# Performance work log

Hardware: AMD Instinct MI355X
Metric: run time of the kernel (lower is better)

The kernel has to match this reference:

```python
import jax, jax.numpy as jnp
import numpy as np
from jax import lax

B, T, D_IN, D_OUT = 8, 4096, 256, 256


def setup_inputs() -> dict:
    key = jax.random.key(0)
    k1, k2, k3, k4, k5 = jax.random.split(key, 5)
    bound_in = 1.0 / np.sqrt(D_IN)
    return {
        "inputs": jax.random.normal(k1, (B, T, D_IN), dtype=jnp.float32),
        "mask": jnp.zeros((B, T, 1), dtype=jnp.float32),
        "W_in": jax.random.uniform(k2, (D_OUT, D_IN), jnp.float32, -bound_in, bound_in),
        "b_in": jax.random.uniform(k3, (D_OUT,), jnp.float32, -bound_in, bound_in),
        "W_f": jax.random.uniform(k4, (D_OUT, D_IN), jnp.float32, -bound_in, bound_in),
        "b_f": jax.random.uniform(k5, (D_OUT,), jnp.float32, -bound_in, bound_in),
    }


def _forget_mult(f, x):
    # h_t = f_t * x_t + (1 - f_t) * h_{t-1}, h_{-1} = 0 (torchqrnn ForgetMult, hidden_init=None)
    fT = jnp.swapaxes(f, 0, 1)  # (T, B, D)
    xT = jnp.swapaxes(x, 0, 1)

    def step(h, fx):
        ft, xt = fx
        h = ft * xt + (1.0 - ft) * h
        return h, h

    h0 = jnp.zeros(xT.shape[1:], dtype=x.dtype)  # (B, D)
    _, hs = lax.scan(step, h0, (fT, xT))
    return jnp.swapaxes(hs, 0, 1)  # (B, T, D)


def reference(inputs, mask, W_in, b_in, W_f, b_f):
    # right_to_left = False -> no flips
    x = jnp.tanh(jnp.einsum("btd,od->bto", inputs, W_in) + b_in)
    f = jax.nn.sigmoid(jnp.einsum("btd,od->bto", inputs, W_f) + b_f + mask * 10000.0)
    return _forget_mult(f, x)
```

## Files before the change

### kernel.cpp

```cpp
#include <hip/hip_runtime.h>
#include <math.h>


typedef _Float16 f16x8 __attribute__((ext_vector_type(8)));
typedef float f32x4 __attribute__((ext_vector_type(4)));
typedef float f32x16 __attribute__((ext_vector_type(16)));
typedef unsigned int u32x4 __attribute__((ext_vector_type(4)));

constexpr int B_ = 8, T_ = 4096, D_ = 256, K_ = 256;
constexpr int M_ = B_ * T_;
constexpr int CHUNK = 64;
constexpr int NCH = T_ / CHUNK;
constexpr int NBLK = M_ / CHUNK;
constexpr int SLICE_EL = 8192;

struct alignas(4) XF { _Float16 x, f; };
struct alignas(4) HP2 { _Float16 h, p; };
union UHP { unsigned int u; HP2 hp; XF xf; };

__device__ __forceinline__ float fexp2(float a) { return __builtin_amdgcn_exp2f(a); }
__device__ __forceinline__ float frcp(float a) { return __builtin_amdgcn_rcpf(a); }
constexpr float L2E = 1.4426950408889634f;

__device__ __forceinline__ float fast_sigmoid(float z) {
  return frcp(1.f + fexp2(-z * L2E));
}
__device__ __forceinline__ float fast_tanh(float z) {
  const float t = fexp2(-2.f * L2E * fabsf(z));
  return copysignf((1.f - t) * frcp(1.f + t), z);
}

__global__ __launch_bounds__(256) void wconv(const float* __restrict__ Win,
                                             const float* __restrict__ Wf,
                                             _Float16* __restrict__ Wh2) {
  const int t = blockIdx.x * 256 + threadIdx.x;
  const int n = t & 255;
  const int kc = (t >> 8) & 1;
  const int mat = (t >> 9) & 1;
  const int kk2 = t >> 10;
  const float* s = (mat ? Wf : Win) + (size_t)n * K_ + kk2 * 16 + kc * 8;
  f32x4 a = *(const f32x4*)s;
  f32x4 b = *(const f32x4*)(s + 4);
  f16x8 o;
  o[0] = (_Float16)a[0]; o[1] = (_Float16)a[1];
  o[2] = (_Float16)a[2]; o[3] = (_Float16)a[3];
  o[4] = (_Float16)b[0]; o[5] = (_Float16)b[1];
  o[6] = (_Float16)b[2]; o[7] = (_Float16)b[3];
  *(f16x8*)(Wh2 + (size_t)t * 8) = o;
}

__global__ __launch_bounds__(256, 3) void gemm_hp(
    const float* __restrict__ A, const _Float16* __restrict__ Wh2,
    const float* __restrict__ bin, const float* __restrict__ bfv,
    const float* __restrict__ mask, unsigned int* __restrict__ HPout,
    float* __restrict__ Ap, float* __restrict__ Hp) {
  __shared__ __align__(16) char smem[32768];
  char* ldsA = smem;

  const int tid = threadIdx.x;
  const int w = tid >> 6, lane = tid & 63;
  const int mw = w >> 1, nw = w & 1;
  const int nl = lane & 31, kh = lane >> 5;
  const int ml = mw * 32 + nl;
  const int g = blockIdx.x;
  const int row0 = g * CHUNK;

  f32x16 acc[2][4];
#pragma unroll
  for (int mat = 0; mat < 2; ++mat)
#pragma unroll
    for (int nt = 0; nt < 4; ++nt) acc[mat][nt] = (f32x16)(0.f);

  {
    const int am = tid >> 2;
    const int ak4 = (tid & 3) * 8;
    const float* agp = A + (size_t)(row0 + am) * K_ + ak4 * 8;
#pragma unroll
    for (int j = 0; j < 8; ++j) {
      const int kcg = ak4 + j;
      f32x4 lo = *(const f32x4*)(agp + j * 8);
      f32x4 hi = *(const f32x4*)(agp + j * 8 + 4);
      f16x8 t;
      t[0] = (_Float16)lo[0]; t[1] = (_Float16)lo[1];
      t[2] = (_Float16)lo[2]; t[3] = (_Float16)lo[3];
      t[4] = (_Float16)hi[0]; t[5] = (_Float16)hi[1];
      t[6] = (_Float16)hi[2]; t[7] = (_Float16)hi[3];
      *(f16x8*)(ldsA + am * 512 + ((kcg ^ (am & 31)) << 4)) = t;
    }
  }
  __syncthreads();

  for (int kk2 = 0; kk2 < 16; ++kk2) {
    f16x8 afr;
    {
      const int kcg = kk2 * 2 + kh;
      afr = *(const f16x8*)(ldsA + ml * 512 + ((kcg ^ (ml & 31)) << 4));
    }
    const _Float16* wslice = Wh2 + (size_t)kk2 * SLICE_EL;
#pragma unroll
    for (int mat = 0; mat < 2; ++mat)
#pragma unroll
      for (int nt = 0; nt < 4; ++nt) {
        const int n = nw * 128 + nt * 32 + nl;
        f16x8 bfr = *(const f16x8*)(wslice + (size_t)((mat * 2 + kh) * 256 + n) * 8);
        acc[mat][nt] = __builtin_amdgcn_mfma_f32_32x32x16_f16(
            afr, bfr, acc[mat][nt], 0, 0, 0);
      }
  }
  __syncthreads();

  float bx[4], bf[4];
#pragma unroll
  for (int nt = 0; nt < 4; ++nt) {
    const int col = nw * 128 + nt * 32 + nl;
    bx[nt] = bin[col];
    bf[nt] = bfv[col];
  }
  float madd[16];
#pragma unroll
  for (int reg = 0; reg < 16; ++reg) {
    const int rl = mw * 32 + (reg & 3) + 8 * (reg >> 2) + 4 * kh;
    madd[reg] = 10000.f * mask[row0 + rl];
  }

  const int d = tid;
  float hrun = 0.f, Prun = 1.f;
#pragma unroll
  for (int p = 0; p < 2; ++p) {
    if (mw == p) {
#pragma unroll
      for (int nt = 0; nt < 4; ++nt) {
        const int col = nw * 128 + nt * 32 + nl;
#pragma unroll
        for (int reg = 0; reg < 16; ++reg) {
          const int rloc = (reg & 3) + 8 * (reg >> 2) + 4 * kh;
          const float zx = acc[0][nt][reg] + bx[nt];
          const float zf = acc[1][nt][reg] + bf[nt] + madd[reg];
          XF v;
          v.x = (_Float16)fast_tanh(zx);
          v.f = (_Float16)fast_sigmoid(zf);
          *(XF*)(smem + ((size_t)rloc * D_ + col) * 4) = v;
        }
      }
    }
    __syncthreads();
#pragma unroll 8
    for (int t = 0; t < 32; ++t) {
      char* slot = smem + ((size_t)t * D_ + d) * 4;
      const XF v = *(const XF*)slot;
      const float f = (float)v.f;
      const float a = 1.f - f;
      hrun = f * (float)v.x + a * hrun;
      Prun *= a;
      HP2 o;
      o.h = (_Float16)hrun;
      o.p = (_Float16)Prun;
      *(HP2*)slot = o;
    }
    __syncthreads();
#pragma unroll
    for (int j = 0; j < 8; ++j) {
      const int c = j * 256 + tid;
      u32x4 vv = *(const u32x4*)(smem + (size_t)c * 16);
      *(u32x4*)(HPout + (size_t)g * 16384 + (size_t)p * 8192 + (size_t)c * 4) = vv;
    }
    __syncthreads();
  }

  Ap[(size_t)g * D_ + d] = Prun;
  Hp[(size_t)g * D_ + d] = hrun;
}

__global__ __launch_bounds__(256) void scan_mid(const float* __restrict__ Ap,
                                                const float* __restrict__ Hp,
                                                float* __restrict__ hs) {
  const int b = blockIdx.x, d = threadIdx.x;
  float h = 0.f;
#pragma unroll 8
  for (int c = 0; c < NCH; ++c) {
    const size_t i = ((size_t)(b * NCH + c)) * D_ + d;
    hs[i] = h;
    h = Hp[i] + Ap[i] * h;
  }
}

__global__ __launch_bounds__(256) void final_k(const unsigned int* __restrict__ HP,
                                               const float* __restrict__ hs,
                                               float* __restrict__ out) {
  const int g = blockIdx.x;
  const int lane = threadIdx.x & 63, wv = threadIdx.x >> 6;
  const int d0 = lane * 4;
  const f32x4 h0 = *(const f32x4*)(hs + (size_t)g * D_ + d0);
#pragma unroll 4
  for (int tt = 0; tt < 16; ++tt) {
    const int t = wv * 16 + tt;
    const size_t idx = ((size_t)g * CHUNK + t) * D_ + d0;
    u32x4 u = *(const u32x4*)(HP + idx);
    f32x4 o;
#pragma unroll
    for (int i = 0; i < 4; ++i) {
      UHP q; q.u = u[i];
      o[i] = (float)q.hp.h + (float)q.hp.p * h0[i];
    }
    *(f32x4*)(out + idx) = o;
  }
}

extern "C" void kernel_launch(void* const* d_in, const int* in_sizes, int n_in,
                              void* d_out, int out_size, void* d_ws, size_t ws_size,
                              hipStream_t stream) {
  const float* inputs = (const float*)d_in[0];
  const float* mask   = (const float*)d_in[1];
  const float* W_in   = (const float*)d_in[2];
  const float* b_in   = (const float*)d_in[3];
  const float* W_f    = (const float*)d_in[4];
  const float* b_f    = (const float*)d_in[5];
  float* out = (float*)d_out;
  char* ws = (char*)d_ws;

  constexpr size_t HPSZ = (size_t)M_ * D_ * 4;
  constexpr size_t WSZ  = (size_t)2 * 256 * 256 * 2;
  constexpr size_t SUM  = (size_t)NBLK * D_ * sizeof(float);

  unsigned int* HPb = (unsigned int*)ws;
  _Float16* Wh2 = (_Float16*)(ws + HPSZ);
  float* Ap = (float*)(ws + HPSZ + WSZ);
  float* Hp = (float*)(ws + HPSZ + WSZ + SUM);
  float* hs = (float*)(ws + HPSZ + WSZ + 2 * SUM);

  wconv<<<64, 256, 0, stream>>>(W_in, W_f, Wh2);
  gemm_hp<<<NBLK, 256, 0, stream>>>(inputs, Wh2, b_in, b_f, mask, HPb, Ap, Hp);
  scan_mid<<<B_, 256, 0, stream>>>(Ap, Hp, hs);
  final_k<<<NBLK, 256, 0, stream>>>(HPb, hs, out);
}
```

Baseline: 151.3 us.

## Fuse GEMM, chunk scan and fixup into one kernel with flag-based lookback

Merges the GEMM/chunk-scan, the cross-chunk scan and the final fixup into one kernel. Each block publishes its chunk carry through global flags, then waits for earlier chunks of the same sequence and recomputes its start state. This removes the large fp16 (h,p) intermediate round-trip through global memory. It also stages weight slices through LDS with register prefetch, and LDS doubles to 64KB, lowering occupancy to 2 blocks per CU. Spin-waiting assumes earlier blocks are scheduled first, which risks deadlock and serialization, and each block re-reads up to 63 prior carries.

Result: slower. 191.8 us (+26.8%).

```diff
diff --git a/kernel.cpp b/kernel.cpp
--- a/kernel.cpp
+++ b/kernel.cpp
@@ -32,8 +32,10 @@
 
 __global__ __launch_bounds__(256) void wconv(const float* __restrict__ Win,
                                              const float* __restrict__ Wf,
-                                             _Float16* __restrict__ Wh2) {
+                                             _Float16* __restrict__ Wh2,
+                                             int* __restrict__ flags) {
   const int t = blockIdx.x * 256 + threadIdx.x;
+  if (t < NBLK) flags[t] = 0;
   const int n = t & 255;
   const int kc = (t >> 8) & 1;
   const int mat = (t >> 9) & 1;
@@ -49,13 +51,15 @@
   *(f16x8*)(Wh2 + (size_t)t * 8) = o;
 }
 
-__global__ __launch_bounds__(256, 3) void gemm_hp(
+__global__ __launch_bounds__(256, 2) void fused(
     const float* __restrict__ A, const _Float16* __restrict__ Wh2,
     const float* __restrict__ bin, const float* __restrict__ bfv,
-    const float* __restrict__ mask, unsigned int* __restrict__ HPout,
-    float* __restrict__ Ap, float* __restrict__ Hp) {
-  __shared__ __align__(16) char smem[32768];
+    const float* __restrict__ mask, float* __restrict__ Ap,
+    float* __restrict__ Hp, int* __restrict__ flags,
+    float* __restrict__ out) {
+  __shared__ __align__(16) char smem[65536];
   char* ldsA = smem;
+  char* ldsW = smem + 32768;
 
   const int tid = threadIdx.x;
   const int w = tid >> 6, lane = tid & 63;
@@ -88,26 +92,40 @@
       *(f16x8*)(ldsA + am * 512 + ((kcg ^ (am & 31)) << 4)) = t;
     }
   }
+
+  f16x8 wreg[4];
+#pragma unroll
+  for (int j = 0; j < 4; ++j)
+    wreg[j] = *(const f16x8*)(Wh2 + (size_t)(j * 256 + tid) * 8);
   __syncthreads();
 
   for (int kk2 = 0; kk2 < 16; ++kk2) {
+#pragma unroll
+    for (int j = 0; j < 4; ++j)
+      *(f16x8*)(ldsW + (size_t)(j * 256 + tid) * 16) = wreg[j];
+    if (kk2 < 15) {
+#pragma unroll
+      for (int j = 0; j < 4; ++j)
+        wreg[j] = *(const f16x8*)(Wh2 + (size_t)(kk2 + 1) * SLICE_EL +
+                                  (size_t)(j * 256 + tid) * 8);
+    }
+    __syncthreads();
     f16x8 afr;
     {
       const int kcg = kk2 * 2 + kh;
       afr = *(const f16x8*)(ldsA + ml * 512 + ((kcg ^ (ml & 31)) << 4));
     }
-    const _Float16* wslice = Wh2 + (size_t)kk2 * SLICE_EL;
 #pragma unroll
     for (int mat = 0; mat < 2; ++mat)
 #pragma unroll
       for (int nt = 0; nt < 4; ++nt) {
         const int n = nw * 128 + nt * 32 + nl;
-        f16x8 bfr = *(const f16x8*)(wslice + (size_t)((mat * 2 + kh) * 256 + n) * 8);
+        f16x8 bfr = *(const f16x8*)(ldsW + (size_t)((mat * 2 + kh) * 256 + n) * 16);
         acc[mat][nt] = __builtin_amdgcn_mfma_f32_32x32x16_f16(
             afr, bfr, acc[mat][nt], 0, 0, 0);
       }
-  }
-  __syncthreads();
+    __syncthreads();
+  }
 
   float bx[4], bf[4];
 #pragma unroll
@@ -123,86 +141,78 @@
     madd[reg] = 10000.f * mask[row0 + rl];
   }
 
+#pragma unroll
+  for (int nt = 0; nt < 4; ++nt) {
+    const int col = nw * 128 + nt * 32 + nl;
+#pragma unroll
+    for (int reg = 0; reg < 16; ++reg) {
+      const int rloc = mw * 32 + (reg & 3) + 8 * (reg >> 2) + 4 * kh;
+      const float zx = acc[0][nt][reg] + bx[nt];
+      const float zf = acc[1][nt][reg] + bf[nt] + madd[reg];
+      XF v;
+      v.x = (_Float16)fast_tanh(zx);
+      v.f = (_Float16)fast_sigmoid(zf);
+      *(XF*)(smem + ((size_t)rloc * D_ + col) * 4) = v;
+    }
+  }
+  __syncthreads();
+
   const int d = tid;
   float hrun = 0.f, Prun = 1.f;
-#pragma unroll
-  for (int p = 0; p < 2; ++p) {
-    if (mw == p) {
-#pragma unroll
-      for (int nt = 0; nt < 4; ++nt) {
-        const int col = nw * 128 + nt * 32 + nl;
-#pragma unroll
-        for (int reg = 0; reg < 16; ++reg) {
-          const int rloc = (reg & 3) + 8 * (reg >> 2) + 4 * kh;
-          const float zx = acc[0][nt][reg] + bx[nt];
-          const float zf = acc[1][nt][reg] + bf[nt] + madd[reg];
-          XF v;
-          v.x = (_Float16)fast_tanh(zx);
-          v.f = (_Float16)fast_sigmoid(zf);
-          *(XF*)(smem + ((size_t)rloc * D_ + col) * 4) = v;
-        }
-      }
-    }
-    __syncthreads();
 #pragma unroll 8
-    for (int t = 0; t < 32; ++t) {
-      char* slot = smem + ((size_t)t * D_ + d) * 4;
-      const XF v = *(const XF*)slot;
-      const float f = (float)v.f;
-      const float a = 1.f - f;
-      hrun = f * (float)v.x + a * hrun;
-      Prun *= a;
-      HP2 o;
-      o.h = (_Float16)hrun;
-      o.p = (_Float16)Prun;
-      *(HP2*)slot = o;
-    }
-    __syncthreads();
-#pragma unroll
-    for (int j = 0; j < 8; ++j) {
-      const int c = j * 256 + tid;
-      u32x4 vv = *(const u32x4*)(smem + (size_t)c * 16);
-      *(u32x4*)(HPout + (size_t)g * 16384 + (size_t)p * 8192 + (size_t)c * 4) = vv;
-    }
-    __syncthreads();
-  }
-
+  for (int t = 0; t < 64; ++t) {
+    char* slot = smem + ((size_t)t * D_ + d) * 4;
+    const XF v = *(const XF*)slot;
+    const float f = (float)v.f;
+    const float a = 1.f - f;
+    hrun = f * (float)v.x + a * hrun;
+    Prun *= a;
+    HP2 o;
+    o.h = (_Float16)hrun;
+    o.p = (_Float16)Prun;
+    *(HP2*)slot = o;
+  }
   Ap[(size_t)g * D_ + d] = Prun;
   Hp[(size_t)g * D_ + d] = hrun;
-}
-
-__global__ __launch_bounds__(256) void scan_mid(const float* __restrict__ Ap,
-                                                const float* __restrict__ Hp,
-                                                float* __restrict__ hs) {
-  const int b = blockIdx.x, d = threadIdx.x;
-  float h = 0.f;
-#pragma unroll 8
-  for (int c = 0; c < NCH; ++c) {
-    const size_t i = ((size_t)(b * NCH + c)) * D_ + d;
-    hs[i] = h;
-    h = Hp[i] + Ap[i] * h;
-  }
-}
-
-__global__ __launch_bounds__(256) void final_k(const unsigned int* __restrict__ HP,
-                                               const float* __restrict__ hs,
-                                               float* __restrict__ out) {
-  const int g = blockIdx.x;
-  const int lane = threadIdx.x & 63, wv = threadIdx.x >> 6;
-  const int d0 = lane * 4;
-  const f32x4 h0 = *(const f32x4*)(hs + (size_t)g * D_ + d0);
+
+  __syncthreads();
+  __threadfence();
+  if (tid == 0)
+    __hip_atomic_store(flags + g, 1, __ATOMIC_RELEASE,
+                       __HIP_MEMORY_SCOPE_AGENT);
+
+  const int c = g & (NCH - 1);
+  const int g0 = g & ~(NCH - 1);
+  if (tid < c) {
+    while (__hip_atomic_load(flags + g0 + tid, __ATOMIC_ACQUIRE,
+                             __HIP_MEMORY_SCOPE_AGENT) == 0)
+      __builtin_amdgcn_s_sleep(2);
+  }
+  __syncthreads();
+  __threadfence();
+
+  const int wv = tid >> 6;
+  const int d0 = (tid & 63) * 4;
+  const size_t seqbase = (size_t)g0 * D_ + d0;
+  f32x4 h0 = (f32x4)(0.f);
+#pragma unroll 4
+  for (int j = 0; j < c; ++j) {
+    const f32x4 a4 = *(const f32x4*)(Ap + seqbase + (size_t)j * D_);
+    const f32x4 hh = *(const f32x4*)(Hp + seqbase + (size_t)j * D_);
+    h0 = hh + a4 * h0;
+  }
+
 #pragma unroll 4
   for (int tt = 0; tt < 16; ++tt) {
     const int t = wv * 16 + tt;
-    const size_t idx = ((size_t)g * CHUNK + t) * D_ + d0;
-    u32x4 u = *(const u32x4*)(HP + idx);
+    const u32x4 u = *(const u32x4*)(smem + ((size_t)t * D_ + d0) * 4);
     f32x4 o;
 #pragma unroll
     for (int i = 0; i < 4; ++i) {
       UHP q; q.u = u[i];
       o[i] = (float)q.hp.h + (float)q.hp.p * h0[i];
     }
-    *(f32x4*)(out + idx) = o;
+    *(f32x4*)(out + ((size_t)(row0 + t)) * D_ + d0) = o;
   }
 }
 
@@ -218,18 +228,15 @@
   float* out = (float*)d_out;
   char* ws = (char*)d_ws;
 
-  constexpr size_t HPSZ = (size_t)M_ * D_ * 4;
-  constexpr size_t WSZ  = (size_t)2 * 256 * 256 * 2;
-  constexpr size_t SUM  = (size_t)NBLK * D_ * sizeof(float);
-
-  unsigned int* HPb = (unsigned int*)ws;
-  _Float16* Wh2 = (_Float16*)(ws + HPSZ);
-  float* Ap = (float*)(ws + HPSZ + WSZ);
-  float* Hp = (float*)(ws + HPSZ + WSZ + SUM);
-  float* hs = (float*)(ws + HPSZ + WSZ + 2 * SUM);
-
-  wconv<<<64, 256, 0, stream>>>(W_in, W_f, Wh2);
-  gemm_hp<<<NBLK, 256, 0, stream>>>(inputs, Wh2, b_in, b_f, mask, HPb, Ap, Hp);
-  scan_mid<<<B_, 256, 0, stream>>>(Ap, Hp, hs);
-  final_k<<<NBLK, 256, 0, stream>>>(HPb, hs, out);
-}
+  constexpr size_t WSZ = (size_t)2 * 256 * 256 * 2;
+  constexpr size_t SUM = (size_t)NBLK * D_ * sizeof(float);
+
+  _Float16* Wh2 = (_Float16*)ws;
+  float* Ap = (float*)(ws + WSZ);
+  float* Hp = (float*)(ws + WSZ + SUM);
+  int* flags = (int*)(ws + WSZ + 2 * SUM);
+
+  wconv<<<64, 256, 0, stream>>>(W_in, W_f, Wh2, flags);
+  fused<<<NBLK, 256, 0, stream>>>(inputs, Wh2, b_in, b_f, mask, Ap, Hp,
+                                  flags, out);
+}
```

## Halve chunk size, stage weights via LDS, fold carry scan into final kernel

Applied to the files above, without the earlier changes.

Shrinks the time chunk from 64 to 32 rows so each GEMM block handles one 32-row tile, with each wave covering 64 output columns. Weight slices are staged through LDS using register prefetch, with occupancy raised to 4 blocks per CU. The separate 8-block serial scan_mid kernel is removed. Each final block instead recomputes its incoming carry by serially combining all previous chunk summaries. That removes a low-parallelism launch but adds redundant work, up to 127 sequential steps in late chunks, plus extra per-slice barriers in the GEMM.

Measured after the change: 140.7 us. -7.0%, faster.

```diff
diff --git a/kernel.cpp b/kernel.cpp
--- a/kernel.cpp
+++ b/kernel.cpp
@@ -9,7 +9,7 @@
 
 constexpr int B_ = 8, T_ = 4096, D_ = 256, K_ = 256;
 constexpr int M_ = B_ * T_;
-constexpr int CHUNK = 64;
+constexpr int CHUNK = 32;
 constexpr int NCH = T_ / CHUNK;
 constexpr int NBLK = M_ / CHUNK;
 constexpr int SLICE_EL = 8192;
@@ -49,34 +49,33 @@
   *(f16x8*)(Wh2 + (size_t)t * 8) = o;
 }
 
-__global__ __launch_bounds__(256, 3) void gemm_hp(
+__global__ __launch_bounds__(256, 4) void gemm_hp(
     const float* __restrict__ A, const _Float16* __restrict__ Wh2,
     const float* __restrict__ bin, const float* __restrict__ bfv,
     const float* __restrict__ mask, unsigned int* __restrict__ HPout,
     float* __restrict__ Ap, float* __restrict__ Hp) {
   __shared__ __align__(16) char smem[32768];
   char* ldsA = smem;
+  char* ldsW = smem + 16384;
 
   const int tid = threadIdx.x;
   const int w = tid >> 6, lane = tid & 63;
-  const int mw = w >> 1, nw = w & 1;
   const int nl = lane & 31, kh = lane >> 5;
-  const int ml = mw * 32 + nl;
   const int g = blockIdx.x;
   const int row0 = g * CHUNK;
 
-  f32x16 acc[2][4];
+  f32x16 acc[2][2];
 #pragma unroll
   for (int mat = 0; mat < 2; ++mat)
 #pragma unroll
-    for (int nt = 0; nt < 4; ++nt) acc[mat][nt] = (f32x16)(0.f);
+    for (int nt = 0; nt < 2; ++nt) acc[mat][nt] = (f32x16)(0.f);
 
   {
-    const int am = tid >> 2;
-    const int ak4 = (tid & 3) * 8;
-    const float* agp = A + (size_t)(row0 + am) * K_ + ak4 * 8;
-#pragma unroll
-    for (int j = 0; j < 8; ++j) {
+    const int am = tid >> 3;
+    const int ak4 = (tid & 7) * 4;
+    const float* agp = A + (size_t)(row0 + am) * K_ + (tid & 7) * 32;
+#pragma unroll
+    for (int j = 0; j < 4; ++j) {
       const int kcg = ak4 + j;
       f32x4 lo = *(const f32x4*)(agp + j * 8);
       f32x4 hi = *(const f32x4*)(agp + j * 8 + 4);
@@ -85,115 +84,124 @@
       t[2] = (_Float16)lo[2]; t[3] = (_Float16)lo[3];
       t[4] = (_Float16)hi[0]; t[5] = (_Float16)hi[1];
       t[6] = (_Float16)hi[2]; t[7] = (_Float16)hi[3];
-      *(f16x8*)(ldsA + am * 512 + ((kcg ^ (am & 31)) << 4)) = t;
-    }
-  }
+      *(f16x8*)(ldsA + am * 512 + ((kcg ^ am) << 4)) = t;
+    }
+  }
+
+  f16x8 wreg[4];
+#pragma unroll
+  for (int j = 0; j < 4; ++j)
+    wreg[j] = *(const f16x8*)(Wh2 + (size_t)(j * 256 + tid) * 8);
   __syncthreads();
 
   for (int kk2 = 0; kk2 < 16; ++kk2) {
+#pragma unroll
+    for (int j = 0; j < 4; ++j)
+      *(f16x8*)(ldsW + (size_t)(j * 256 + tid) * 16) = wreg[j];
+    if (kk2 < 15) {
+#pragma unroll
+      for (int j = 0; j < 4; ++j)
+        wreg[j] = *(const f16x8*)(Wh2 + (size_t)(kk2 + 1) * SLICE_EL +
+                                  (size_t)(j * 256 + tid) * 8);
+    }
+    __syncthreads();
     f16x8 afr;
     {
       const int kcg = kk2 * 2 + kh;
-      afr = *(const f16x8*)(ldsA + ml * 512 + ((kcg ^ (ml & 31)) << 4));
-    }
-    const _Float16* wslice = Wh2 + (size_t)kk2 * SLICE_EL;
+      afr = *(const f16x8*)(ldsA + nl * 512 + ((kcg ^ nl) << 4));
+    }
 #pragma unroll
     for (int mat = 0; mat < 2; ++mat)
 #pragma unroll
-      for (int nt = 0; nt < 4; ++nt) {
-        const int n = nw * 128 + nt * 32 + nl;
-        f16x8 bfr = *(const f16x8*)(wslice + (size_t)((mat * 2 + kh) * 256 + n) * 8);
+      for (int nt = 0; nt < 2; ++nt) {
+        const int n = w * 64 + nt * 32 + nl;
+        f16x8 bfr = *(const f16x8*)(ldsW + (size_t)((mat * 2 + kh) * 256 + n) * 16);
         acc[mat][nt] = __builtin_amdgcn_mfma_f32_32x32x16_f16(
             afr, bfr, acc[mat][nt], 0, 0, 0);
       }
-  }
-  __syncthreads();
-
-  float bx[4], bf[4];
-#pragma unroll
-  for (int nt = 0; nt < 4; ++nt) {
-    const int col = nw * 128 + nt * 32 + nl;
+    __syncthreads();
+  }
+
+  float bx[2], bf[2];
+#pragma unroll
+  for (int nt = 0; nt < 2; ++nt) {
+    const int col = w * 64 + nt * 32 + nl;
     bx[nt] = bin[col];
     bf[nt] = bfv[col];
   }
   float madd[16];
 #pragma unroll
   for (int reg = 0; reg < 16; ++reg) {
-    const int rl = mw * 32 + (reg & 3) + 8 * (reg >> 2) + 4 * kh;
+    const int rl = (reg & 3) + 8 * (reg >> 2) + 4 * kh;
     madd[reg] = 10000.f * mask[row0 + rl];
   }
+
+#pragma unroll
+  for (int nt = 0; nt < 2; ++nt) {
+    const int col = w * 64 + nt * 32 + nl;
+#pragma unroll
+    for (int reg = 0; reg < 16; ++reg) {
+      const int rloc = (reg & 3) + 8 * (reg >> 2) + 4 * kh;
+      const float zx = acc[0][nt][reg] + bx[nt];
+      const float zf = acc[1][nt][reg] + bf[nt] + madd[reg];
+      XF v;
+      v.x = (_Float16)fast_tanh(zx);
+      v.f = (_Float16)fast_sigmoid(zf);
+      *(XF*)(smem + ((size_t)rloc * D_ + col) * 4) = v;
+    }
+  }
+  __syncthreads();
 
   const int d = tid;
   float hrun = 0.f, Prun = 1.f;
-#pragma unroll
-  for (int p = 0; p < 2; ++p) {
-    if (mw == p) {
-#pragma unroll
-      for (int nt = 0; nt < 4; ++nt) {
-        const int col = nw * 128 + nt * 32 + nl;
-#pragma unroll
-        for (int reg = 0; reg < 16; ++reg) {
-          const int rloc = (reg & 3) + 8 * (reg >> 2) + 4 * kh;
-          const float zx = acc[0][nt][reg] + bx[nt];
-          const float zf = acc[1][nt][reg] + bf[nt] + madd[reg];
-          XF v;
-          v.x = (_Float16)fast_tanh(zx);
-          v.f = (_Float16)fast_sigmoid(zf);
-          *(XF*)(smem + ((size_t)rloc * D_ + col) * 4) = v;
-        }
-      }
-    }
-    __syncthreads();
 #pragma unroll 8
-    for (int t = 0; t < 32; ++t) {
-      char* slot = smem + ((size_t)t * D_ + d) * 4;
-      const XF v = *(const XF*)slot;
-      const float f = (float)v.f;
-      const float a = 1.f - f;
-      hrun = f * (float)v.x + a * hrun;
-      Prun *= a;
-      HP2 o;
-      o.h = (_Float16)hrun;
-      o.p = (_Float16)Prun;
-      *(HP2*)slot = o;
-    }
-    __syncthreads();
-#pragma unroll
-    for (int j = 0; j < 8; ++j) {
-      const int c = j * 256 + tid;
-      u32x4 vv = *(const u32x4*)(smem + (size_t)c * 16);
-      *(u32x4*)(HPout + (size_t)g * 16384 + (size_t)p * 8192 + (size_t)c * 4) = vv;
-    }
-    __syncthreads();
+  for (int t = 0; t < 32; ++t) {
+    char* slot = smem + ((size_t)t * D_ + d) * 4;
+    const XF v = *(const XF*)slot;
+    const float f = (float)v.f;
+    const float a = 1.f - f;
+    hrun = f * (float)v.x + a * hrun;
+    Prun *= a;
+    HP2 o;
+    o.h = (_Float16)hrun;
+    o.p = (_Float16)Prun;
+    *(HP2*)slot = o;
+  }
+  __syncthreads();
+
+#pragma unroll
+  for (int j = 0; j < 8; ++j) {
+    const int c = j * 256 + tid;
+    u32x4 vv = *(const u32x4*)(smem + (size_t)c * 16);
+    *(u32x4*)(HPout + (size_t)g * 8192 + (size_t)c * 4) = vv;
   }
 
   Ap[(size_t)g * D_ + d] = Prun;
   Hp[(size_t)g * D_ + d] = hrun;
 }
 
-__global__ __launch_bounds__(256) void scan_mid(const float* __restrict__ Ap,
-                                                const float* __restrict__ Hp,
-                                                float* __restrict__ hs) {
-  const int b = blockIdx.x, d = threadIdx.x;
-  float h = 0.f;
-#pragma unroll 8
-  for (int c = 0; c < NCH; ++c) {
-    const size_t i = ((size_t)(b * NCH + c)) * D_ + d;
-    hs[i] = h;
-    h = Hp[i] + Ap[i] * h;
-  }
-}
-
 __global__ __launch_bounds__(256) void final_k(const unsigned int* __restrict__ HP,
-                                               const float* __restrict__ hs,
+                                               const float* __restrict__ Ap,
+                                               const float* __restrict__ Hp,
                                                float* __restrict__ out) {
   const int g = blockIdx.x;
-  const int lane = threadIdx.x & 63, wv = threadIdx.x >> 6;
-  const int d0 = lane * 4;
-  const f32x4 h0 = *(const f32x4*)(hs + (size_t)g * D_ + d0);
+  const int c = g & (NCH - 1);
+  const int g0 = g & ~(NCH - 1);
+  const int wv = threadIdx.x >> 6;
+  const int d0 = (threadIdx.x & 63) * 4;
+
+  const size_t seqbase = (size_t)g0 * D_ + d0;
+  f32x4 h0 = (f32x4)(0.f);
 #pragma unroll 4
-  for (int tt = 0; tt < 16; ++tt) {
-    const int t = wv * 16 + tt;
+  for (int j = 0; j < c; ++j) {
+    const f32x4 a4 = *(const f32x4*)(Ap + seqbase + (size_t)j * D_);
+    const f32x4 hh = *(const f32x4*)(Hp + seqbase + (size_t)j * D_);
+    h0 = hh + a4 * h0;
+  }
+
+#pragma unroll 4
+  for (int tt = 0; tt < 8; ++tt) {
+    const int t = wv * 8 + tt;
     const size_t idx = ((size_t)g * CHUNK + t) * D_ + d0;
     u32x4 u = *(const u32x4*)(HP + idx);
     f32x4 o;
@@ -226,10 +234,8 @@
   _Float16* Wh2 = (_Float16*)(ws + HPSZ);
   float* Ap = (float*)(ws + HPSZ + WSZ);
   float* Hp = (float*)(ws + HPSZ + WSZ + SUM);
-  float* hs = (float*)(ws + HPSZ + WSZ + 2 * SUM);
 
   wconv<<<64, 256, 0, stream>>>(W_in, W_f, Wh2);
   gemm_hp<<<NBLK, 256, 0, stream>>>(inputs, Wh2, b_in, b_f, mask, HPb, Ap, Hp);
-  scan_mid<<<B_, 256, 0, stream>>>(Ap, Hp, hs);
-  final_k<<<NBLK, 256, 0, stream>>>(HPb, hs, out);
-}
+  final_k<<<NBLK, 256, 0, stream>>>(HPb, Ap, Hp, out);
+}
```
